# Performance work log

Hardware: AMD Instinct MI355X
Metric: run time of the kernel (lower is better)

## Reference

```python
import jax, jax.numpy as jnp
from jax import lax
import numpy as np

T = 49        # number of timesteps (hard-coded in source)
UNITS = 256
QN = 9        # n_basis of the Fourier expansion
DIM = 256     # input feature dim
BATCH = 2048
SQRT2 = float(np.sqrt(2.0))


def fourier_basis(q, t):
    """skfda Fourier basis on domain (0,1): [1, sqrt2*sin(2pi t), sqrt2*cos(2pi t), ...].
    t: (T,) -> (T, q). Assumes q odd (constant + (q-1)/2 sin/cos pairs)."""
    cols = [jnp.ones_like(t)]
    for i in range(1, (q - 1) // 2 + 1):
        w = 2.0 * np.pi * i
        cols.append(SQRT2 * jnp.sin(w * t))
        cols.append(SQRT2 * jnp.cos(w * t))
    return jnp.stack(cols, axis=-1)


def setup_inputs() -> dict:
    key = jax.random.key(0)
    ks = jax.random.split(key, 6)
    cat_dim = DIM + UNITS
    return {
        "x": jax.random.normal(ks[0], (BATCH, T, DIM), dtype=jnp.float32),
        "Wf": jax.random.normal(ks[1], (cat_dim, UNITS), dtype=jnp.float32) * 0.05,
        "Wi": jax.random.normal(ks[2], (cat_dim, UNITS), dtype=jnp.float32) * 0.05,
        "Wc": jax.random.normal(ks[3], (cat_dim, UNITS), dtype=jnp.float32) * 0.05,
        "Wo": jax.random.normal(ks[4], (cat_dim, UNITS), dtype=jnp.float32) * 0.05,
        "Q": jax.random.normal(ks[5], (UNITS, QN * UNITS), dtype=jnp.float32) * 0.05,
    }


def reference(x, Wf, Wi, Wc, Wo, Q):
    # Per-step Fourier basis values Bt (T, q).  block_diag(Bt,...,Bt).T against Q
    # is equivalent to contracting Q.reshape(units, units, q) with Bt.
    tgrid = jnp.linspace(0.0, 1.0, T)
    B = fourier_basis(QN, tgrid)                              # (T, q)
    Qr = Q.reshape(UNITS, UNITS, QN)
    U = jnp.einsum('ijq,tq->tij', Qr, B)                      # (T, units, units)

    def step(c, inp):
        xt, Ut = inp                                          # (B, D), (units, units)
        cat = jnp.concatenate([c, xt], axis=-1)               # Ht := states[0] == c
        f = jax.nn.sigmoid(cat @ Wf)
        i = jax.nn.sigmoid(cat @ Wi)
        g = jax.nn.sigmoid(cat @ Wc)                          # sigmoid, as in source
        c_new = i * g + f * c                                 # Ct := states[0] == c
        o = jnp.tanh(cat @ Wo)                                # tanh, as in source
        s = o * jnp.tanh(c_new)
        h = jnp.tanh(s @ Ut)                                  # time-varying projection
        return c_new, h

    c0 = jnp.zeros((x.shape[0], UNITS), dtype=x.dtype)
    _, hs = lax.scan(step, c0, (jnp.swapaxes(x, 0, 1), U))    # hs: (T, B, units)
    return jnp.swapaxes(hs, 0, 1)                             # (B, T, units)
```

## Files before the change

kernel.cpp:

```cpp
#include <hip/hip_runtime.h>


typedef unsigned short u16;
typedef unsigned int u32;
typedef __attribute__((ext_vector_type(8))) short bf16x8;
typedef __attribute__((ext_vector_type(4))) float f32x4;

#define T_STEPS 49
#define OUT_ROW 12544

__device__ __forceinline__ u16 f2b(float f) {
  u32 u = __float_as_uint(f);
  u += 0x7fffu + ((u >> 16) & 1u);
  return (u16)(u >> 16);
}
__device__ __forceinline__ float b2f(u16 h) { return __uint_as_float(((u32)h) << 16); }
__device__ __forceinline__ float sigm(float z) { return 1.0f / (1.0f + __expf(-z)); }
__device__ __forceinline__ float tanh_f(float z) {
  float e = __expf(-2.0f * fabsf(z));
  float r = (1.0f - e) / (1.0f + e);
  return __builtin_copysignf(r, z);
}

__global__ void pack_w(const float* __restrict__ Wf, const float* __restrict__ Wi,
                       const float* __restrict__ Wc, const float* __restrict__ Wo,
                       u16* __restrict__ WcP, u16* __restrict__ WxP) {
  int n = blockIdx.x, k = threadIdx.x;
  int g = n >> 8, u = n & 255;
  const float* W = (g == 0) ? Wf : (g == 1) ? Wi : (g == 2) ? Wc : Wo;
  WcP[n * 256 + k] = f2b(W[k * 256 + u]);
  WxP[n * 256 + k] = f2b(W[(256 + k) * 256 + u]);
}

__global__ void pack_u(const float* __restrict__ Q, u16* __restrict__ UP) {
  int bx = blockIdx.x;
  int t = bx >> 8, jp = bx & 255, j = threadIdx.x;
  const float* q = Q + j * 2304 + jp * 9;
  float tv = (float)t / 48.0f;
  float acc = q[0];
  const float SQ2 = 1.41421356237f;
#pragma unroll
  for (int i = 1; i <= 4; ++i) {
    float ang = 6.283185307179586f * (float)i * tv;
    acc += SQ2 * (sinf(ang) * q[2 * i - 1] + cosf(ang) * q[2 * i]);
  }
  UP[t * 65536 + jp * 256 + j] = f2b(acc);
}

__global__ __launch_bounds__(512) void xproj_k(const float* __restrict__ x,
                                               const u16* __restrict__ WxP,
                                               u16* __restrict__ xp,
                                               int t0, int ct) {
  __shared__ u16 aLds[64][264];
  int tid = threadIdx.x;
  int m0 = blockIdx.x * 64;
#pragma unroll
  for (int it = 0; it < 8; ++it) {
    int flat = it * 2048 + tid * 4;
    int r = flat >> 8, k = flat & 255;
    int rg = m0 + r;
    int b = rg / ct;
    int tt = rg - b * ct;
    const f32x4 v = __builtin_nontemporal_load(
        (const f32x4*)&x[(b * T_STEPS + (t0 + tt)) * 256 + k]);
    u16 tmp[4] = {f2b(v.x), f2b(v.y), f2b(v.z), f2b(v.w)};
    *(uint2*)&aLds[r][k] = *(uint2*)tmp;
  }
  __syncthreads();
  int w = tid >> 6, l = tid & 63, lane15 = l & 15, quad = l >> 4;
  for (int rtp = 0; rtp < 2; ++rtp) {
    bf16x8 af[2][8];
#pragma unroll
    for (int h = 0; h < 2; ++h)
#pragma unroll
      for (int ks = 0; ks < 8; ++ks)
        af[h][ks] = *(const bf16x8*)&aLds[rtp * 32 + h * 16 + lane15][ks * 32 + quad * 8];
    for (int ctl = 0; ctl < 8; ++ctl) {
      const u16* bp = WxP + (w * 128 + ctl * 16 + lane15) * 256 + quad * 8;
      bf16x8 bf[8];
#pragma unroll
      for (int ks = 0; ks < 8; ++ks) bf[ks] = *(const bf16x8*)(bp + ks * 32);
#pragma unroll
      for (int h = 0; h < 2; ++h) {
        f32x4 acc = {0.f, 0.f, 0.f, 0.f};
#pragma unroll
        for (int ks = 0; ks < 8; ++ks)
          acc = __builtin_amdgcn_mfma_f32_16x16x32_bf16(af[h][ks], bf[ks], acc, 0, 0, 0);
        int col = w * 128 + ctl * 16 + lane15;
        int rloc = rtp * 32 + h * 16 + quad * 4;
#pragma unroll
        for (int i = 0; i < 4; ++i)
          __builtin_nontemporal_store(f2b(acc[i]), &xp[(m0 + rloc + i) * 1024 + col]);
      }
    }
  }
}

__global__ __launch_bounds__(1024) void rec_k(const u16* __restrict__ WcP,
                                              const u16* __restrict__ UP,
                                              const u16* __restrict__ xp,
                                              float* __restrict__ out,
                                              float* __restrict__ cstate,
                                              int tA, int tB, int cc) {
  __shared__ float cF[8][256];
  __shared__ u16 cB[16][264];
  __shared__ u16 sB[16][264];
  __shared__ float Z[8][1024];
  int tid = threadIdx.x;
  int b0 = blockIdx.x * 8;
  for (int i = tid; i < 16 * 264; i += 1024) {
    ((u16*)cB)[i] = 0;
    ((u16*)sB)[i] = 0;
  }
  for (int i = tid; i < 2048; i += 1024) {
    int r = i >> 8, u = i & 255;
    float c0 = (tA == 0) ? 0.0f : cstate[(b0 + r) * 256 + u];
    cF[r][u] = c0;
    cB[r][u] = f2b(c0);
  }
  __syncthreads();
  int w = tid >> 6, l = tid & 63, lane15 = l & 15, quad = l >> 4;

#pragma unroll 1
  for (int t = tA; t < tB; ++t) {
    u16 xpv[2][4];
#pragma unroll
    for (int p = 0; p < 2; ++p) {
      int idx = tid + p * 1024;
      int r = idx >> 8, u = idx & 255;
      const u16* xb = xp + ((b0 + r) * cc + (t - tA)) * 1024 + u;
#pragma unroll
      for (int g = 0; g < 4; ++g) xpv[p][g] = __builtin_nontemporal_load(xb + g * 256);
    }
    bf16x8 af[8];
#pragma unroll
    for (int ks = 0; ks < 8; ++ks)
      af[ks] = *(const bf16x8*)&cB[lane15][ks * 32 + quad * 8];
#pragma unroll
    for (int c8 = 0; c8 < 4; ++c8) {
      f32x4 acc = {0.f, 0.f, 0.f, 0.f};
      const u16* bp = WcP + (w * 64 + c8 * 16 + lane15) * 256 + quad * 8;
#pragma unroll
      for (int ks = 0; ks < 8; ++ks)
        acc = __builtin_amdgcn_mfma_f32_16x16x32_bf16(af[ks], *(const bf16x8*)(bp + ks * 32), acc, 0, 0, 0);
      if (quad < 2) {
        int col = w * 64 + c8 * 16 + lane15;
#pragma unroll
        for (int i = 0; i < 4; ++i) Z[quad * 4 + i][col] = acc[i];
      }
    }
    __syncthreads();
#pragma unroll
    for (int p = 0; p < 2; ++p) {
      int idx = tid + p * 1024;
      int r = idx >> 8, u = idx & 255;
      float zf = Z[r][u] + b2f(xpv[p][0]);
      float zi = Z[r][256 + u] + b2f(xpv[p][1]);
      float zg = Z[r][512 + u] + b2f(xpv[p][2]);
      float zo = Z[r][768 + u] + b2f(xpv[p][3]);
      float f = sigm(zf), ii = sigm(zi), gg = sigm(zg), o = tanh_f(zo);
      float cn = ii * gg + f * cF[r][u];
      cF[r][u] = cn;
      cB[r][u] = f2b(cn);
      float s = o * tanh_f(cn);
      sB[r][u] = f2b(s);
    }
    __syncthreads();
    bf16x8 sf[8];
#pragma unroll
    for (int ks = 0; ks < 8; ++ks)
      sf[ks] = *(const bf16x8*)&sB[lane15][ks * 32 + quad * 8];
    {
      f32x4 acc = {0.f, 0.f, 0.f, 0.f};
      const u16* up = UP + t * 65536 + (w * 16 + lane15) * 256 + quad * 8;
#pragma unroll
      for (int ks = 0; ks < 8; ++ks)
        acc = __builtin_amdgcn_mfma_f32_16x16x32_bf16(sf[ks], *(const bf16x8*)(up + ks * 32), acc, 0, 0, 0);
      if (quad < 2) {
        int col = w * 16 + lane15;
#pragma unroll
        for (int i = 0; i < 4; ++i)
          __builtin_nontemporal_store(
              tanh_f(acc[i]), &out[(b0 + quad * 4 + i) * OUT_ROW + t * 256 + col]);
      }
    }
  }
  if (tB < T_STEPS) {
    for (int i = tid; i < 2048; i += 1024) {
      int r = i >> 8, u = i & 255;
      cstate[(b0 + r) * 256 + u] = cF[r][u];
    }
  }
}

extern "C" void kernel_launch(void* const* d_in, const int* in_sizes, int n_in,
                              void* d_out, int out_size, void* d_ws, size_t ws_size,
                              hipStream_t stream) {
  const float* x = (const float*)d_in[0];
  const float* Wf = (const float*)d_in[1];
  const float* Wi = (const float*)d_in[2];
  const float* Wc = (const float*)d_in[3];
  const float* Wo = (const float*)d_in[4];
  const float* Q = (const float*)d_in[5];
  float* out = (float*)d_out;

  char* p = (char*)d_ws;
  u16* WcP = (u16*)p;           p += (size_t)1024 * 256 * 2;
  u16* WxP = (u16*)p;           p += (size_t)1024 * 256 * 2;
  u16* UP = (u16*)p;            p += (size_t)49 * 256 * 256 * 2;
  float* cstate = (float*)p;    p += (size_t)2048 * 256 * 4;
  u16* xpb = (u16*)p;
  size_t used = (size_t)(p - (char*)d_ws);
  size_t rem = (ws_size > used) ? (ws_size - used) : 0;
  const size_t perT = (size_t)2048 * 1024 * 2;
  int CT = (int)(rem / perT);
  if (CT > 49) CT = 49;
  if (CT < 1) CT = 1;

  pack_w<<<dim3(1024), dim3(256), 0, stream>>>(Wf, Wi, Wc, Wo, WcP, WxP);
  pack_u<<<dim3(49 * 256), dim3(256), 0, stream>>>(Q, UP);

  for (int t0 = 0; t0 < T_STEPS; t0 += CT) {
    int cc = (T_STEPS - t0 < CT) ? (T_STEPS - t0) : CT;
    xproj_k<<<dim3(2048 * cc / 64), dim3(512), 0, stream>>>(x, WxP, xpb, t0, cc);
    rec_k<<<dim3(256), dim3(1024), 0, stream>>>(WcP, UP, xpb, out, cstate, t0, t0 + cc, cc);
  }
}
```

Baseline: 1.203 ms.

## Fuse input projection into recurrence and defer time-varying output projection

Drops the separate x-projection pass and its bf16 intermediate. The recurrent kernel now does one K=512 GEMM over [c, x_t], with x_{t+1} prefetched into a double-buffered, XOR-swizzled LDS tile and the cell state held in registers. The s @ U_t projection and tanh move out of the serial loop into a separate fully parallel kernel over all timesteps, which reads a stored s buffer. This removes two barriers per step and the Z staging, at the cost of a 49x2048x256 bf16 intermediate, and it uses only 128 blocks for the recurrence, which may underfill the GPU.

```diff
diff --git a/kernel.cpp b/kernel.cpp
--- a/kernel.cpp
+++ b/kernel.cpp
@@ -24,12 +24,12 @@
 
 __global__ void pack_w(const float* __restrict__ Wf, const float* __restrict__ Wi,
                        const float* __restrict__ Wc, const float* __restrict__ Wo,
-                       u16* __restrict__ WcP, u16* __restrict__ WxP) {
+                       u16* __restrict__ WP) {
   int n = blockIdx.x, k = threadIdx.x;
   int g = n >> 8, u = n & 255;
   const float* W = (g == 0) ? Wf : (g == 1) ? Wi : (g == 2) ? Wc : Wo;
-  WcP[n * 256 + k] = f2b(W[k * 256 + u]);
-  WxP[n * 256 + k] = f2b(W[(256 + k) * 256 + u]);
+  WP[n * 512 + k] = f2b(W[k * 256 + u]);
+  WP[n * 512 + 256 + k] = f2b(W[(256 + k) * 256 + u]);
 }
 
 __global__ void pack_u(const float* __restrict__ Q, u16* __restrict__ UP) {
@@ -47,148 +47,118 @@
   UP[t * 65536 + jp * 256 + j] = f2b(acc);
 }
 
-__global__ __launch_bounds__(512) void xproj_k(const float* __restrict__ x,
-                                               const u16* __restrict__ WxP,
-                                               u16* __restrict__ xp,
-                                               int t0, int ct) {
-  __shared__ u16 aLds[64][264];
+__global__ __launch_bounds__(1024) void rec_k(const u16* __restrict__ WP,
+                                              const float* __restrict__ x,
+                                              u16* __restrict__ S) {
+  __shared__ u16 aB[2][16 * 512];
   int tid = threadIdx.x;
-  int m0 = blockIdx.x * 64;
-#pragma unroll
-  for (int it = 0; it < 8; ++it) {
-    int flat = it * 2048 + tid * 4;
-    int r = flat >> 8, k = flat & 255;
-    int rg = m0 + r;
-    int b = rg / ct;
-    int tt = rg - b * ct;
+  int b0 = blockIdx.x * 16;
+  int w = tid >> 6, l = tid & 63, lane15 = l & 15, quad = l >> 4;
+  int u_own = w * 16 + lane15;
+
+  int sr = tid >> 6;
+  int sc = (tid & 63) * 4;
+
+  {
+    uint2 z2 = {0u, 0u};
+    int bc = sc * 2;
+    *(uint2*)((char*)&aB[0][0] + sr * 1024 + (bc ^ ((sr & 7) << 4))) = z2;
     const f32x4 v = __builtin_nontemporal_load(
-        (const f32x4*)&x[(b * T_STEPS + (t0 + tt)) * 256 + k]);
+        (const f32x4*)&x[((size_t)(b0 + sr) * T_STEPS + 0) * 256 + sc]);
     u16 tmp[4] = {f2b(v.x), f2b(v.y), f2b(v.z), f2b(v.w)};
-    *(uint2*)&aLds[r][k] = *(uint2*)tmp;
+    int bx2 = 512 + sc * 2;
+    *(uint2*)((char*)&aB[0][0] + sr * 1024 + (bx2 ^ ((sr & 7) << 4))) = *(uint2*)tmp;
   }
   __syncthreads();
+
+  float creg[4] = {0.f, 0.f, 0.f, 0.f};
+  const u16* bp0 = WP + ((size_t)(0 * 256 + u_own)) * 512 + quad * 8;
+  const u16* bp1 = WP + ((size_t)(1 * 256 + u_own)) * 512 + quad * 8;
+  const u16* bp2 = WP + ((size_t)(2 * 256 + u_own)) * 512 + quad * 8;
+  const u16* bp3 = WP + ((size_t)(3 * 256 + u_own)) * 512 + quad * 8;
+  u16* Sl = S + (size_t)(b0 + quad * 4) * 256 + u_own;
+
+  int p = 0;
+#pragma unroll 1
+  for (int t = 0; t < T_STEPS; ++t) {
+    f32x4 xv = {0.f, 0.f, 0.f, 0.f};
+    if (t + 1 < T_STEPS)
+      xv = __builtin_nontemporal_load(
+          (const f32x4*)&x[((size_t)(b0 + sr) * T_STEPS + (t + 1)) * 256 + sc]);
+
+    f32x4 a0 = {0.f, 0.f, 0.f, 0.f}, a1 = a0, a2 = a0, a3 = a0;
+    const char* ab = (const char*)&aB[p][0];
+#pragma unroll
+    for (int ks = 0; ks < 16; ++ks) {
+      bf16x8 af = *(const bf16x8*)(ab + lane15 * 1024 +
+                                   ((ks * 64 + quad * 16) ^ ((lane15 & 7) << 4)));
+      a0 = __builtin_amdgcn_mfma_f32_16x16x32_bf16(af, *(const bf16x8*)(bp0 + ks * 32), a0, 0, 0, 0);
+      a1 = __builtin_amdgcn_mfma_f32_16x16x32_bf16(af, *(const bf16x8*)(bp1 + ks * 32), a1, 0, 0, 0);
+      a2 = __builtin_amdgcn_mfma_f32_16x16x32_bf16(af, *(const bf16x8*)(bp2 + ks * 32), a2, 0, 0, 0);
+      a3 = __builtin_amdgcn_mfma_f32_16x16x32_bf16(af, *(const bf16x8*)(bp3 + ks * 32), a3, 0, 0, 0);
+    }
+
+    char* abn = (char*)&aB[p ^ 1][0];
+#pragma unroll
+    for (int i = 0; i < 4; ++i) {
+      int r = quad * 4 + i;
+      float f = sigm(a0[i]), ii = sigm(a1[i]), gg = sigm(a2[i]), o = tanh_f(a3[i]);
+      float cn = ii * gg + f * creg[i];
+      creg[i] = cn;
+      if (t + 1 < T_STEPS)
+        *(u16*)(abn + r * 1024 + ((u_own * 2) ^ ((r & 7) << 4))) = f2b(cn);
+      float s = o * tanh_f(cn);
+      Sl[((size_t)t * 2048 + i) * 256] = f2b(s);
+    }
+
+    if (t + 1 < T_STEPS) {
+      u16 tmp[4] = {f2b(xv.x), f2b(xv.y), f2b(xv.z), f2b(xv.w)};
+      int bx2 = 512 + sc * 2;
+      *(uint2*)(abn + sr * 1024 + (bx2 ^ ((sr & 7) << 4))) = *(uint2*)tmp;
+    }
+    __syncthreads();
+    p ^= 1;
+  }
+}
+
+__global__ __launch_bounds__(512) void proj_k(const u16* __restrict__ S,
+                                              const u16* __restrict__ UP,
+                                              float* __restrict__ out) {
+  int bx = blockIdx.x;
+  int t = bx >> 5, mt = bx & 31;
+  int m0 = mt * 64;
+  int tid = threadIdx.x;
   int w = tid >> 6, l = tid & 63, lane15 = l & 15, quad = l >> 4;
+  const u16* Sbase = S + ((size_t)t * 2048 + m0) * 256;
+  const u16* Ubase = UP + (size_t)t * 65536;
+#pragma unroll
   for (int rtp = 0; rtp < 2; ++rtp) {
     bf16x8 af[2][8];
 #pragma unroll
     for (int h = 0; h < 2; ++h)
 #pragma unroll
       for (int ks = 0; ks < 8; ++ks)
-        af[h][ks] = *(const bf16x8*)&aLds[rtp * 32 + h * 16 + lane15][ks * 32 + quad * 8];
-    for (int ctl = 0; ctl < 8; ++ctl) {
-      const u16* bp = WxP + (w * 128 + ctl * 16 + lane15) * 256 + quad * 8;
+        af[h][ks] = *(const bf16x8*)(Sbase + (rtp * 32 + h * 16 + lane15) * 256 +
+                                     ks * 32 + quad * 8);
+#pragma unroll
+    for (int ct = 0; ct < 2; ++ct) {
+      int col = w * 32 + ct * 16 + lane15;
+      const u16* up = Ubase + col * 256 + quad * 8;
       bf16x8 bf[8];
 #pragma unroll
-      for (int ks = 0; ks < 8; ++ks) bf[ks] = *(const bf16x8*)(bp + ks * 32);
+      for (int ks = 0; ks < 8; ++ks) bf[ks] = *(const bf16x8*)(up + ks * 32);
 #pragma unroll
       for (int h = 0; h < 2; ++h) {
         f32x4 acc = {0.f, 0.f, 0.f, 0.f};
 #pragma unroll
         for (int ks = 0; ks < 8; ++ks)
           acc = __builtin_amdgcn_mfma_f32_16x16x32_bf16(af[h][ks], bf[ks], acc, 0, 0, 0);
-        int col = w * 128 + ctl * 16 + lane15;
-        int rloc = rtp * 32 + h * 16 + quad * 4;
 #pragma unroll
-        for (int i = 0; i < 4; ++i)
-          __builtin_nontemporal_store(f2b(acc[i]), &xp[(m0 + rloc + i) * 1024 + col]);
+        for (int i = 0; i < 4; ++i) {
+          int b = m0 + rtp * 32 + h * 16 + quad * 4 + i;
+          out[(size_t)b * OUT_ROW + t * 256 + col] = tanh_f(acc[i]);
+        }
       }
-    }
-  }
-}
-
-__global__ __launch_bounds__(1024) void rec_k(const u16* __restrict__ WcP,
-                                              const u16* __restrict__ UP,
-                                              const u16* __restrict__ xp,
-                                              float* __restrict__ out,
-                                              float* __restrict__ cstate,
-                                              int tA, int tB, int cc) {
-  __shared__ float cF[8][256];
-  __shared__ u16 cB[16][264];
-  __shared__ u16 sB[16][264];
-  __shared__ float Z[8][1024];
-  int tid = threadIdx.x;
-  int b0 = blockIdx.x * 8;
-  for (int i = tid; i < 16 * 264; i += 1024) {
-    ((u16*)cB)[i] = 0;
-    ((u16*)sB)[i] = 0;
-  }
-  for (int i = tid; i < 2048; i += 1024) {
-    int r = i >> 8, u = i & 255;
-    float c0 = (tA == 0) ? 0.0f : cstate[(b0 + r) * 256 + u];
-    cF[r][u] = c0;
-    cB[r][u] = f2b(c0);
-  }
-  __syncthreads();
-  int w = tid >> 6, l = tid & 63, lane15 = l & 15, quad = l >> 4;
-
-#pragma unroll 1
-  for (int t = tA; t < tB; ++t) {
-    u16 xpv[2][4];
-#pragma unroll
-    for (int p = 0; p < 2; ++p) {
-      int idx = tid + p * 1024;
-      int r = idx >> 8, u = idx & 255;
-      const u16* xb = xp + ((b0 + r) * cc + (t - tA)) * 1024 + u;
-#pragma unroll
-      for (int g = 0; g < 4; ++g) xpv[p][g] = __builtin_nontemporal_load(xb + g * 256);
-    }
-    bf16x8 af[8];
-#pragma unroll
-    for (int ks = 0; ks < 8; ++ks)
-      af[ks] = *(const bf16x8*)&cB[lane15][ks * 32 + quad * 8];
-#pragma unroll
-    for (int c8 = 0; c8 < 4; ++c8) {
-      f32x4 acc = {0.f, 0.f, 0.f, 0.f};
-      const u16* bp = WcP + (w * 64 + c8 * 16 + lane15) * 256 + quad * 8;
-#pragma unroll
-      for (int ks = 0; ks < 8; ++ks)
-        acc = __builtin_amdgcn_mfma_f32_16x16x32_bf16(af[ks], *(const bf16x8*)(bp + ks * 32), acc, 0, 0, 0);
-      if (quad < 2) {
-        int col = w * 64 + c8 * 16 + lane15;
-#pragma unroll
-        for (int i = 0; i < 4; ++i) Z[quad * 4 + i][col] = acc[i];
-      }
-    }
-    __syncthreads();
-#pragma unroll
-    for (int p = 0; p < 2; ++p) {
-      int idx = tid + p * 1024;
-      int r = idx >> 8, u = idx & 255;
-      float zf = Z[r][u] + b2f(xpv[p][0]);
-      float zi = Z[r][256 + u] + b2f(xpv[p][1]);
-      float zg = Z[r][512 + u] + b2f(xpv[p][2]);
-      float zo = Z[r][768 + u] + b2f(xpv[p][3]);
-      float f = sigm(zf), ii = sigm(zi), gg = sigm(zg), o = tanh_f(zo);
-      float cn = ii * gg + f * cF[r][u];
-      cF[r][u] = cn;
-      cB[r][u] = f2b(cn);
-      float s = o * tanh_f(cn);
-      sB[r][u] = f2b(s);
-    }
-    __syncthreads();
-    bf16x8 sf[8];
-#pragma unroll
-    for (int ks = 0; ks < 8; ++ks)
-      sf[ks] = *(const bf16x8*)&sB[lane15][ks * 32 + quad * 8];
-    {
-      f32x4 acc = {0.f, 0.f, 0.f, 0.f};
-      const u16* up = UP + t * 65536 + (w * 16 + lane15) * 256 + quad * 8;
-#pragma unroll
-      for (int ks = 0; ks < 8; ++ks)
-        acc = __builtin_amdgcn_mfma_f32_16x16x32_bf16(sf[ks], *(const bf16x8*)(up + ks * 32), acc, 0, 0, 0);
-      if (quad < 2) {
-        int col = w * 16 + lane15;
-#pragma unroll
-        for (int i = 0; i < 4; ++i)
-          __builtin_nontemporal_store(
-              tanh_f(acc[i]), &out[(b0 + quad * 4 + i) * OUT_ROW + t * 256 + col]);
-      }
-    }
-  }
-  if (tB < T_STEPS) {
-    for (int i = tid; i < 2048; i += 1024) {
-      int r = i >> 8, u = i & 255;
-      cstate[(b0 + r) * 256 + u] = cF[r][u];
     }
   }
 }
@@ -205,24 +175,13 @@
   float* out = (float*)d_out;
 
   char* p = (char*)d_ws;
-  u16* WcP = (u16*)p;           p += (size_t)1024 * 256 * 2;
-  u16* WxP = (u16*)p;           p += (size_t)1024 * 256 * 2;
-  u16* UP = (u16*)p;            p += (size_t)49 * 256 * 256 * 2;
-  float* cstate = (float*)p;    p += (size_t)2048 * 256 * 4;
-  u16* xpb = (u16*)p;
-  size_t used = (size_t)(p - (char*)d_ws);
-  size_t rem = (ws_size > used) ? (ws_size - used) : 0;
-  const size_t perT = (size_t)2048 * 1024 * 2;
-  int CT = (int)(rem / perT);
-  if (CT > 49) CT = 49;
-  if (CT < 1) CT = 1;
+  u16* WP = (u16*)p;  p += (size_t)1024 * 512 * 2;
+  u16* UP = (u16*)p;  p += (size_t)49 * 256 * 256 * 2;
+  u16* Sb = (u16*)p;  p += (size_t)49 * 2048 * 256 * 2;
+  (void)ws_size;
 
-  pack_w<<<dim3(1024), dim3(256), 0, stream>>>(Wf, Wi, Wc, Wo, WcP, WxP);
+  pack_w<<<dim3(1024), dim3(256), 0, stream>>>(Wf, Wi, Wc, Wo, WP);
   pack_u<<<dim3(49 * 256), dim3(256), 0, stream>>>(Q, UP);
-
-  for (int t0 = 0; t0 < T_STEPS; t0 += CT) {
-    int cc = (T_STEPS - t0 < CT) ? (T_STEPS - t0) : CT;
-    xproj_k<<<dim3(2048 * cc / 64), dim3(512), 0, stream>>>(x, WxP, xpb, t0, cc);
-    rec_k<<<dim3(256), dim3(1024), 0, stream>>>(WcP, UP, xpb, out, cstate, t0, t0 + cc, cc);
-  }
+  rec_k<<<dim3(128), dim3(1024), 0, stream>>>(WP, x, Sb);
+  proj_k<<<dim3(49 * 32), dim3(512), 0, stream>>>(Sb, UP, out);
 }
```

Result: slower. 1.510 ms (+25.5%).
